# Kernel optimization log

Measured on AMD Instinct MI355X. Metric: run time of the kernel, lower is better.

The kernel has to match this reference:

```python
import jax, jax.numpy as jnp
import numpy as np

N_NODES, N_EDGES, MAX_NB = 40000, 80000, 4
INPUT_SIZE, NODE_FDIM, HIDDEN = 384, 256, 256
DEPTH = 6


def setup_inputs() -> dict:
    key = jax.random.key(0)
    ks = jax.random.split(key, 16)
    s = 0.05  # weight init scale
    return {
        "fnode": jax.random.normal(ks[0], (N_NODES, NODE_FDIM), dtype=jnp.float32),
        "fmess": jax.random.normal(ks[1], (N_EDGES, INPUT_SIZE), dtype=jnp.float32),
        "agraph": jax.random.randint(ks[2], (N_NODES, MAX_NB), 0, N_EDGES),
        "bgraph": jax.random.randint(ks[3], (N_EDGES, MAX_NB), 0, N_EDGES),
        "mask": jnp.ones((N_NODES, 1), dtype=jnp.float32),
        "Wz": jax.random.normal(ks[4], (INPUT_SIZE + HIDDEN, HIDDEN), dtype=jnp.float32) * s,
        "bz": jnp.zeros((HIDDEN,), dtype=jnp.float32),
        "Wr": jax.random.normal(ks[5], (INPUT_SIZE, HIDDEN), dtype=jnp.float32) * s,
        "Ur": jax.random.normal(ks[6], (HIDDEN, HIDDEN), dtype=jnp.float32) * s,
        "bur": jnp.zeros((HIDDEN,), dtype=jnp.float32),
        "Wh": jax.random.normal(ks[7], (INPUT_SIZE + HIDDEN, HIDDEN), dtype=jnp.float32) * s,
        "bh": jnp.zeros((HIDDEN,), dtype=jnp.float32),
        "Wo": jax.random.normal(ks[8], (NODE_FDIM + HIDDEN, HIDDEN), dtype=jnp.float32) * s,
        "bo": jnp.zeros((HIDDEN,), dtype=jnp.float32),
        "depth": DEPTH,
    }


def reference(fnode, fmess, agraph, bgraph, mask, Wz, bz, Wr, Ur, bur, Wh, bh, Wo, bo, depth):
    E, H = fmess.shape[0], Wz.shape[1]
    # message 0 is padding -> kept at zero each step (mask[0,0]=0 in torch GRU)
    msg_mask = jnp.ones((E, 1), dtype=fmess.dtype).at[0, 0].set(0.0)
    rx = fmess @ Wr  # precomputable: [E, H], reset gate input term

    def step(h, _):
        h_nei = h[bgraph]                      # [E, nb, H] gather
        sum_h = h_nei.sum(axis=1)              # [E, H]
        z = jax.nn.sigmoid(jnp.concatenate([fmess, sum_h], axis=1) @ Wz + bz)
        r = jax.nn.sigmoid(rx[:, None, :] + h_nei @ Ur + bur)  # [E, nb, H]
        sum_gh = (r * h_nei).sum(axis=1)
        pre_h = jnp.tanh(jnp.concatenate([fmess, sum_gh], axis=1) @ Wh + bh)
        h_new = ((1.0 - z) * sum_h + z * pre_h) * msg_mask
        return h_new, None

    h0 = jnp.zeros((E, H), dtype=fmess.dtype)
    h, _ = jax.lax.scan(step, h0, None, length=depth)

    nei_message = h[agraph].sum(axis=1)        # [N, H] gather-sum over incoming edges
    node_hiddens = jax.nn.relu(jnp.concatenate([fnode, nei_message], axis=1) @ Wo + bo)
    return node_hiddens * mask, h
```

## Files before the change

### kernel.cpp

```cpp
#include <hip/hip_runtime.h>
#include <stdint.h>

#define N_NODES 40000
#define N_EDGES 80000
#define HID 256
#define HC_LD 512
#define DEPTH_FIXED 6
#define NPAD 40064
#define MT 16

typedef __bf16 bf16;
typedef __bf16 bf16x4 __attribute__((ext_vector_type(4)));
typedef __bf16 bf16x8 __attribute__((ext_vector_type(8)));
typedef float f32x4 __attribute__((ext_vector_type(4)));

#define TPAD 136
#define APAD 264

__device__ __forceinline__ float sigmoidf_(float x) { return 1.f / (1.f + __expf(-x)); }
__device__ __forceinline__ float tanhf_(float x) { float e = __expf(2.f * x); return 1.f - 2.f / (e + 1.f); }

__device__ __forceinline__ void gld_lds16(const void* g, void* l) {
    __builtin_amdgcn_global_load_lds(
        (const __attribute__((address_space(1))) uint32_t*)g,
        (__attribute__((address_space(3))) uint32_t*)l, 16, 0, 0);
}

__device__ __forceinline__ void stage_tile(const bf16* __restrict__ src, int ld, int r0, int k0,
                                           bf16* lds, int tid) {
#pragma unroll
    for (int jj = 0; jj < 2; ++jj) {
        int s = jj * 256 + tid;
        int c = s ^ ((s >> 3) & 3);
        gld_lds16(src + (size_t)(r0 + (c >> 2)) * ld + k0 + (c & 3) * 8, lds + s * 8);
    }
}

__device__ __forceinline__ void mfma_tile(const bf16* lds_a, const bf16* lds_b,
                                          int wm, int wn, int lane, f32x4 (&acc)[4][4]) {
    const int li = lane & 15, quad = lane >> 4;
    const int sw = quad ^ ((li >> 1) & 3);
    bf16x8 a[4], b[4];
#pragma unroll
    for (int i = 0; i < 4; ++i)
        a[i] = *(const bf16x8*)(lds_a + ((wm * 64 + i * 16 + li) * 4 + sw) * 8);
#pragma unroll
    for (int j = 0; j < 4; ++j)
        b[j] = *(const bf16x8*)(lds_b + ((wn * 64 + j * 16 + li) * 4 + sw) * 8);
#pragma unroll
    for (int i = 0; i < 4; ++i)
#pragma unroll
        for (int j = 0; j < 4; ++j)
            acc[i][j] = __builtin_amdgcn_mfma_f32_16x16x32_bf16(a[i], b[j], acc[i][j], 0, 0, 0);
}

__global__ __launch_bounds__(256, 3) void step_fused_k(
    const int* __restrict__ bgraph, const bf16* __restrict__ HC,
    const bf16* __restrict__ P,
    const bf16* __restrict__ B1T, const bf16* __restrict__ B2T,
    bf16* __restrict__ HCn, float* __restrict__ HF) {
    __shared__ __align__(16) bf16 sA1[MT * APAD];
    __shared__ __align__(16) bf16 sA2[MT * APAD];
    __shared__ __align__(16) bf16 sBst[2 * 8192];
    const int tid = threadIdx.x, lane = tid & 63, wave = tid >> 6;
    const int m0 = blockIdx.x * MT;
    const int li = lane & 15, quad = lane >> 4;

#pragma unroll
    for (int v = 0; v < 2; ++v) {
#pragma unroll
        for (int jj = 0; jj < 4; ++jj) {
            int s = wave * 256 + jj * 64 + lane;
            int c = s ^ ((s >> 3) & 3);
            gld_lds16(B1T + (size_t)(c >> 2) * 256 + v * 32 + (c & 3) * 8,
                      sBst + v * 8192 + s * 8);
        }
    }

    {
        const int r = tid >> 4, qc = tid & 15;
        const int e = m0 + r;
        const int4 nb = *(const int4*)(bgraph + (size_t)e * 4);
        const int bi[4] = {nb.x, nb.y, nb.z, nb.w};
        const bf16* prx = P + (size_t)e * 768 + qc * 16;
        bf16x8 rx[2];
        rx[0] = *(const bf16x8*)(prx);
        rx[1] = *(const bf16x8*)(prx + 8);
        float sh[2][8] = {}, gh[2][8] = {};
#pragma unroll
        for (int p = 0; p < 2; ++p) {
            bf16x8 hv[2][2], uv[2][2];
#pragma unroll
            for (int jj = 0; jj < 2; ++jj) {
                const bf16* hp = HC + (size_t)bi[p * 2 + jj] * HC_LD + qc * 16;
                hv[jj][0] = *(const bf16x8*)(hp);
                hv[jj][1] = *(const bf16x8*)(hp + 8);
                uv[jj][0] = *(const bf16x8*)(hp + 256);
                uv[jj][1] = *(const bf16x8*)(hp + 256 + 8);
            }
#pragma unroll
            for (int jj = 0; jj < 2; ++jj)
#pragma unroll
                for (int c = 0; c < 2; ++c)
#pragma unroll
                    for (int u = 0; u < 8; ++u) {
                        float hf = (float)hv[jj][c][u];
                        float rr = sigmoidf_((float)rx[c][u] + (float)uv[jj][c][u]);
                        sh[c][u] += hf;
                        gh[c][u] += rr * hf;
                    }
        }
#pragma unroll
        for (int c = 0; c < 2; ++c) {
            bf16x8 os, og;
#pragma unroll
            for (int u = 0; u < 8; ++u) { os[u] = (bf16)sh[c][u]; og[u] = (bf16)gh[c][u]; }
            *(bf16x8*)(sA1 + r * APAD + qc * 16 + c * 8) = os;
            *(bf16x8*)(sA2 + r * APAD + qc * 16 + c * 8) = og;
        }
    }
    __syncthreads();

    const int sw = quad ^ ((li >> 1) & 3);
    f32x4 accZ[4] = {}, accH[4] = {};
#pragma unroll
    for (int u = 0; u < 16; ++u) {
        if (u < 15) { asm volatile("s_waitcnt vmcnt(4)" ::: "memory"); }
        else        { asm volatile("s_waitcnt vmcnt(0)" ::: "memory"); }
        __builtin_amdgcn_sched_barrier(0);
        const bf16* sA = (u < 8) ? sA1 : sA2;
        const int t = u & 7;
        bf16x8 a = *(const bf16x8*)(sA + li * APAD + t * 32 + quad * 8);
        bf16x8 b[4];
#pragma unroll
        for (int j = 0; j < 4; ++j)
            b[j] = *(const bf16x8*)(sBst + (u & 1) * 8192 + ((wave * 64 + j * 16 + li) * 4 + sw) * 8);
        asm volatile("s_waitcnt lgkmcnt(0)" ::: "memory");
        __builtin_amdgcn_sched_barrier(0);
        const int v = u + 2;
        if (v < 16) {
            const bf16* BTn = (v < 8) ? B1T : B2T;
            const int tn = v & 7;
#pragma unroll
            for (int jj = 0; jj < 4; ++jj) {
                int s = wave * 256 + jj * 64 + lane;
                int c = s ^ ((s >> 3) & 3);
                gld_lds16(BTn + (size_t)(c >> 2) * 256 + tn * 32 + (c & 3) * 8,
                          sBst + (u & 1) * 8192 + s * 8);
            }
        }
#pragma unroll
        for (int j = 0; j < 4; ++j) {
            if (u < 8) accZ[j] = __builtin_amdgcn_mfma_f32_16x16x32_bf16(a, b[j], accZ[j], 0, 0, 0);
            else       accH[j] = __builtin_amdgcn_mfma_f32_16x16x32_bf16(a, b[j], accH[j], 0, 0, 0);
        }
    }

    __syncthreads();

    bf16* tZ = sA2;
    bf16* tH = sBst;
#pragma unroll
    for (int j = 0; j < 4; ++j) {
        const int col = wave * 64 + j * 16 + li;
#pragma unroll
        for (int r = 0; r < 4; ++r) {
            const int row = quad * 4 + r;
            tZ[row * APAD + col] = (bf16)accZ[j][r];
            tH[row * 256 + col] = (bf16)accH[j][r];
        }
    }
    __syncthreads();
#pragma unroll
    for (int s = 0; s < 2; ++s) {
        int v = s * 256 + tid;
        int lr = v >> 5, c8 = (v & 31) * 8;
        int e = m0 + lr;
        bf16x8 zl = *(const bf16x8*)(tZ + lr * APAD + c8);
        bf16x8 hl = *(const bf16x8*)(tH + lr * 256 + c8);
        bf16x8 shv = *(const bf16x8*)(sA1 + lr * APAD + c8);
        bf16x8 zx = *(const bf16x8*)(P + (size_t)e * 768 + 256 + c8);
        bf16x8 hx = *(const bf16x8*)(P + (size_t)e * 768 + 512 + c8);
        bf16x8 o;
        float of[8];
#pragma unroll
        for (int u = 0; u < 8; ++u) {
            float z = sigmoidf_((float)zl[u] + (float)zx[u]);
            float p = tanhf_((float)hl[u] + (float)hx[u]);
            float hn = (1.f - z) * (float)shv[u] + z * p;
            if (e == 0) hn = 0.f;
            o[u] = (bf16)hn;
            of[u] = hn;
        }
        *(bf16x8*)(HCn + (size_t)e * HC_LD + c8) = o;
        if (HF) {
            *(float4*)(HF + (size_t)e * HID + c8) = make_float4(of[0], of[1], of[2], of[3]);
            *(float4*)(HF + (size_t)e * HID + c8 + 4) = make_float4(of[4], of[5], of[6], of[7]);
        }
    }
}

__global__ __launch_bounds__(256) void gemm_single_k(
    const bf16* __restrict__ A, int lda, const bf16* __restrict__ BT,
    const float* __restrict__ bias, bf16* __restrict__ C, int K, int ldc) {
    __shared__ __align__(16) char smem[34816];
    bf16* sA = (bf16*)smem;
    bf16* sB = sA + 4096;
    const int tid = threadIdx.x, lane = tid & 63, wave = tid >> 6;
    const int wm = wave >> 1, wn = wave & 1;
    const int m0 = blockIdx.x * 128, n0 = blockIdx.y * 128;
    f32x4 acc[4][4] = {};
    for (int k0 = 0; k0 < K; k0 += 32) {
        stage_tile(A, lda, m0, k0, sA, tid);
        stage_tile(BT, K, n0, k0, sB, tid);
        __syncthreads();
        mfma_tile(sA, sB, wm, wn, lane, acc);
        __syncthreads();
    }
    bf16* tC = (bf16*)smem;
#pragma unroll
    for (int i = 0; i < 4; ++i)
#pragma unroll
        for (int j = 0; j < 4; ++j) {
            const int col = wn * 64 + j * 16 + (lane & 15);
#pragma unroll
            for (int r = 0; r < 4; ++r) {
                const int lr = wm * 64 + i * 16 + (lane >> 4) * 4 + r;
                tC[lr * TPAD + col] = (bf16)acc[i][j][r];
            }
        }
    __syncthreads();
#pragma unroll
    for (int s = 0; s < 8; ++s) {
        int v = s * 256 + tid;
        int lr = v >> 4, c8 = (v & 15) * 8;
        bf16x8 cv = *(const bf16x8*)(tC + lr * TPAD + c8);
        bf16x8 o;
        if (bias) {
            float4 b0 = *(const float4*)(bias + n0 + c8);
            float4 b1 = *(const float4*)(bias + n0 + c8 + 4);
            o[0] = (bf16)((float)cv[0] + b0.x); o[1] = (bf16)((float)cv[1] + b0.y);
            o[2] = (bf16)((float)cv[2] + b0.z); o[3] = (bf16)((float)cv[3] + b0.w);
            o[4] = (bf16)((float)cv[4] + b1.x); o[5] = (bf16)((float)cv[5] + b1.y);
            o[6] = (bf16)((float)cv[6] + b1.z); o[7] = (bf16)((float)cv[7] + b1.w);
        } else {
            o = cv;
        }
        *(bf16x8*)(C + (size_t)(m0 + lr) * ldc + n0 + c8) = o;
    }
}

__global__ __launch_bounds__(256) void gemm_out_k(
    const bf16* __restrict__ A1, const bf16* __restrict__ A2,
    const bf16* __restrict__ B1T, const bf16* __restrict__ B2T,
    const float* __restrict__ bo, const float* __restrict__ mask, float* __restrict__ out) {
    __shared__ __align__(16) char smem[34816];
    bf16* s0 = (bf16*)smem;
    bf16* s1 = s0 + 4096;
    bf16* s2 = s1 + 4096;
    bf16* s3 = s2 + 4096;
    const int tid = threadIdx.x, lane = tid & 63, wave = tid >> 6;
    const int wm = wave >> 1, wn = wave & 1;
    const int m0 = blockIdx.x * 128, n0 = blockIdx.y * 128;
    f32x4 acc1[4][4] = {}, acc2[4][4] = {};
    for (int k0 = 0; k0 < 256; k0 += 32) {
        stage_tile(A1, 256, m0, k0, s0, tid);
        stage_tile(B1T, 256, n0, k0, s1, tid);
        stage_tile(A2, 256, m0, k0, s2, tid);
        stage_tile(B2T, 256, n0, k0, s3, tid);
        __syncthreads();
        mfma_tile(s0, s1, wm, wn, lane, acc1);
        mfma_tile(s2, s3, wm, wn, lane, acc2);
        __syncthreads();
    }
    bf16* tC = (bf16*)smem;
#pragma unroll
    for (int i = 0; i < 4; ++i)
#pragma unroll
        for (int j = 0; j < 4; ++j) {
            const int col = wn * 64 + j * 16 + (lane & 15);
#pragma unroll
            for (int r = 0; r < 4; ++r) {
                const int lr = wm * 64 + i * 16 + (lane >> 4) * 4 + r;
                tC[lr * TPAD + col] = (bf16)(acc1[i][j][r] + acc2[i][j][r]);
            }
        }
    __syncthreads();
#pragma unroll
    for (int s = 0; s < 8; ++s) {
        int v = s * 256 + tid;
        int lr = v >> 4, c8 = (v & 15) * 8;
        int grow = m0 + lr;
        if (grow >= N_NODES) continue;
        int gcol = n0 + c8;
        bf16x8 cv = *(const bf16x8*)(tC + lr * TPAD + c8);
        float4 b0 = *(const float4*)(bo + gcol);
        float4 b1 = *(const float4*)(bo + gcol + 4);
        float mk = mask[grow];
        float4 o0, o1;
        o0.x = fmaxf((float)cv[0] + b0.x, 0.f) * mk;
        o0.y = fmaxf((float)cv[1] + b0.y, 0.f) * mk;
        o0.z = fmaxf((float)cv[2] + b0.z, 0.f) * mk;
        o0.w = fmaxf((float)cv[3] + b0.w, 0.f) * mk;
        o1.x = fmaxf((float)cv[4] + b1.x, 0.f) * mk;
        o1.y = fmaxf((float)cv[5] + b1.y, 0.f) * mk;
        o1.z = fmaxf((float)cv[6] + b1.z, 0.f) * mk;
        o1.w = fmaxf((float)cv[7] + b1.w, 0.f) * mk;
        *(float4*)(out + (size_t)grow * 256 + gcol) = o0;
        *(float4*)(out + (size_t)grow * 256 + gcol + 4) = o1;
    }
}

__global__ __launch_bounds__(256) void gather_nei_k(
    const int* __restrict__ agraph, const bf16* __restrict__ H, bf16* __restrict__ nei) {
    int i = blockIdx.x * 256 + threadIdx.x;
    int v = i >> 5, c8 = (i & 31) * 8;
    bf16x8 o;
    if (v < N_NODES) {
        int4 nb = *(const int4*)(agraph + (size_t)v * 4);
        int bi[4] = {nb.x, nb.y, nb.z, nb.w};
        float s[8] = {};
#pragma unroll
        for (int j = 0; j < 4; ++j) {
            bf16x8 hv = *(const bf16x8*)(H + (size_t)bi[j] * HC_LD + c8);
#pragma unroll
            for (int r = 0; r < 8; ++r) s[r] += (float)hv[r];
        }
#pragma unroll
        for (int r = 0; r < 8; ++r) o[r] = (bf16)s[r];
    } else {
#pragma unroll
        for (int r = 0; r < 8; ++r) o[r] = (bf16)0.f;
    }
    *(bf16x8*)(nei + (size_t)v * HID + c8) = o;
}

__global__ __launch_bounds__(256) void step1_k(const bf16* __restrict__ P, bf16* __restrict__ HC) {
    int i = blockIdx.x * 256 + threadIdx.x;
    int e = i >> 5, c8 = (i & 31) * 8;
    bf16x8 zx = *(const bf16x8*)(P + (size_t)e * 768 + 256 + c8);
    bf16x8 hx = *(const bf16x8*)(P + (size_t)e * 768 + 512 + c8);
    bf16x8 o;
#pragma unroll
    for (int r = 0; r < 8; ++r) {
        float h = sigmoidf_((float)zx[r]) * tanhf_((float)hx[r]);
        if (e == 0) h = 0.f;
        o[r] = (bf16)h;
    }
    *(bf16x8*)(HC + (size_t)e * HC_LD + c8) = o;
}

__global__ void cvt_bf16_k(const float* __restrict__ src, bf16* __restrict__ dst, int n4) {
    int i = blockIdx.x * 256 + threadIdx.x;
    if (i >= n4) return;
    float4 v = ((const float4*)src)[i];
    bf16x4 o = {(bf16)v.x, (bf16)v.y, (bf16)v.z, (bf16)v.w};
    *((bf16x4*)dst + i) = o;
}

__global__ void cvt_fnode_k(const float* __restrict__ src, bf16* __restrict__ dst) {
    int i = blockIdx.x * 256 + threadIdx.x;
    int row = i >> 6;
    bf16x4 o = {(bf16)0.f, (bf16)0.f, (bf16)0.f, (bf16)0.f};
    if (row < N_NODES) {
        float4 v = ((const float4*)src)[i];
        o[0] = (bf16)v.x; o[1] = (bf16)v.y; o[2] = (bf16)v.z; o[3] = (bf16)v.w;
    }
    *((bf16x4*)dst + i) = o;
}

__global__ void prep_wpre_k(const float* __restrict__ Wr, const float* __restrict__ Wz,
                            const float* __restrict__ Wh, bf16* __restrict__ WT) {
    int idx = blockIdx.x * 256 + threadIdx.x;
    if (idx >= 768 * 384) return;
    int n = idx / 384, k = idx % 384;
    float v;
    if (n < 256) v = Wr[(size_t)k * 256 + n];
    else if (n < 512) v = Wz[(size_t)k * 256 + (n - 256)];
    else v = Wh[(size_t)k * 256 + (n - 512)];
    WT[idx] = (bf16)v;
}

__global__ void prep_bias_k(const float* __restrict__ bur, const float* __restrict__ bz,
                            const float* __restrict__ bh, float* __restrict__ bp) {
    int n = blockIdx.x * 256 + threadIdx.x;
    if (n >= 768) return;
    bp[n] = n < 256 ? bur[n] : (n < 512 ? bz[n - 256] : bh[n - 512]);
}

__global__ void prep_t256_k(const float* __restrict__ W, bf16* __restrict__ T, int roff) {
    int idx = blockIdx.x * 256 + threadIdx.x;
    int n = idx >> 8, k = idx & 255;
    T[idx] = (bf16)W[(size_t)(roff + k) * 256 + n];
}

extern "C" void kernel_launch(void* const* d_in, const int* in_sizes, int n_in,
                              void* d_out, int out_size, void* d_ws, size_t ws_size,
                              hipStream_t stream) {
    (void)in_sizes; (void)n_in; (void)out_size; (void)ws_size;
    const float* fnode = (const float*)d_in[0];
    const float* fmess = (const float*)d_in[1];
    const int* agraph = (const int*)d_in[2];
    const int* bgraph = (const int*)d_in[3];
    const float* mask = (const float*)d_in[4];
    const float* Wz = (const float*)d_in[5];
    const float* bz = (const float*)d_in[6];
    const float* Wr = (const float*)d_in[7];
    const float* Ur = (const float*)d_in[8];
    const float* bur = (const float*)d_in[9];
    const float* Wh = (const float*)d_in[10];
    const float* bh = (const float*)d_in[11];
    const float* Wo = (const float*)d_in[12];
    const float* bo = (const float*)d_in[13];
    float* out_node = (float*)d_out;
    float* out_h = out_node + (size_t)N_NODES * HID;

    char* ws = (char*)d_ws;
    size_t off = 0;
    auto alloc = [&](size_t b) -> char* { char* p = ws + off; off += (b + 255) & ~(size_t)255; return p; };
    bf16* P     = (bf16*)alloc((size_t)N_EDGES * 768 * 2);
    bf16* HC0   = (bf16*)alloc((size_t)N_EDGES * HC_LD * 2);
    bf16* HC1   = (bf16*)alloc((size_t)N_EDGES * HC_LD * 2);
    bf16* fnodeB= (bf16*)alloc((size_t)NPAD * HID * 2);
    bf16* nei   = (bf16*)alloc((size_t)NPAD * HID * 2);
    bf16* WTpre = (bf16*)alloc((size_t)768 * 384 * 2);
    bf16* UrT   = (bf16*)alloc(65536 * 2);
    bf16* WzBT  = (bf16*)alloc(65536 * 2);
    bf16* WhBT  = (bf16*)alloc(65536 * 2);
    bf16* WoTT  = (bf16*)alloc(65536 * 2);
    bf16* WoBT  = (bf16*)alloc(65536 * 2);
    float* biasP= (float*)alloc(768 * 4);
    bf16* fmessB = HC1;

    cvt_bf16_k<<<30000, 256, 0, stream>>>(fmess, fmessB, N_EDGES * 384 / 4);
    cvt_fnode_k<<<NPAD * 64 / 256, 256, 0, stream>>>(fnode, fnodeB);
    prep_wpre_k<<<(768 * 384 + 255) / 256, 256, 0, stream>>>(Wr, Wz, Wh, WTpre);
    prep_bias_k<<<3, 256, 0, stream>>>(bur, bz, bh, biasP);
    prep_t256_k<<<256, 256, 0, stream>>>(Ur, UrT, 0);
    prep_t256_k<<<256, 256, 0, stream>>>(Wz, WzBT, 384);
    prep_t256_k<<<256, 256, 0, stream>>>(Wh, WhBT, 384);
    prep_t256_k<<<256, 256, 0, stream>>>(Wo, WoTT, 0);
    prep_t256_k<<<256, 256, 0, stream>>>(Wo, WoBT, 256);

    gemm_single_k<<<dim3(625, 6), 256, 0, stream>>>(fmessB, 384, WTpre, biasP, P, 384, 768);

    step1_k<<<N_EDGES * 32 / 256, 256, 0, stream>>>(P, HC0);

    bf16* cur = HC0;
    bf16* nxt = HC1;
    for (int d = 2; d <= DEPTH_FIXED; ++d) {
        gemm_single_k<<<dim3(625, 2), 256, 0, stream>>>(cur, HC_LD, UrT, nullptr, cur + 256, 256, HC_LD);
        step_fused_k<<<N_EDGES / MT, 256, 0, stream>>>(bgraph, cur, P, WzBT, WhBT, nxt,
                                                       d == DEPTH_FIXED ? out_h : nullptr);
        bf16* t = cur; cur = nxt; nxt = t;
    }

    gather_nei_k<<<NPAD * 32 / 256, 256, 0, stream>>>(agraph, cur, nei);
    gemm_out_k<<<dim3(313, 2), 256, 0, stream>>>(fnodeB, nei, WoTT, WoBT, bo, mask, out_node);
}
```

Before: 1.232 ms.

## Double step kernel edge tile to 32 rows with 8 waves per block

The fused GRU step kernel now processes 32 edges per block with 512 threads. Each of the 8 waves owns a 32-column slice and computes a 2x2 grid of MFMA tiles, so every weight tile streamed into shared memory is reused across twice as many edges. The neighbour gather now issues all four neighbour row loads before any arithmetic, which raises memory-level parallelism. In exchange it uses more registers, and the larger blocks may lower occupancy and leave fewer blocks to spread across the GPU.

```diff
diff --git a/kernel.cpp b/kernel.cpp
--- a/kernel.cpp
+++ b/kernel.cpp
@@ -7,7 +7,7 @@
 #define HC_LD 512
 #define DEPTH_FIXED 6
 #define NPAD 40064
-#define MT 16
+#define MT 32
 
 typedef __bf16 bf16;
 typedef __bf16 bf16x4 __attribute__((ext_vector_type(4)));
@@ -54,7 +54,7 @@
             acc[i][j] = __builtin_amdgcn_mfma_f32_16x16x32_bf16(a[i], b[j], acc[i][j], 0, 0, 0);
 }
 
-__global__ __launch_bounds__(256, 3) void step_fused_k(
+__global__ __launch_bounds__(512, 2) void step_fused_k(
     const int* __restrict__ bgraph, const bf16* __restrict__ HC,
     const bf16* __restrict__ P,
     const bf16* __restrict__ B1T, const bf16* __restrict__ B2T,
@@ -69,11 +69,11 @@
 #pragma unroll
     for (int v = 0; v < 2; ++v) {
 #pragma unroll
-        for (int jj = 0; jj < 4; ++jj) {
-            int s = wave * 256 + jj * 64 + lane;
+        for (int jj = 0; jj < 2; ++jj) {
+            int s = jj * 64 + lane;
             int c = s ^ ((s >> 3) & 3);
-            gld_lds16(B1T + (size_t)(c >> 2) * 256 + v * 32 + (c & 3) * 8,
-                      sBst + v * 8192 + s * 8);
+            gld_lds16(B1T + (size_t)(wave * 32 + (c >> 2)) * 256 + v * 32 + (c & 3) * 8,
+                      sBst + v * 8192 + wave * 1024 + s * 8);
         }
     }
 
@@ -86,30 +86,27 @@
         bf16x8 rx[2];
         rx[0] = *(const bf16x8*)(prx);
         rx[1] = *(const bf16x8*)(prx + 8);
+        bf16x8 hv[4][2], uv[4][2];
+#pragma unroll
+        for (int j = 0; j < 4; ++j) {
+            const bf16* hp = HC + (size_t)bi[j] * HC_LD + qc * 16;
+            hv[j][0] = *(const bf16x8*)(hp);
+            hv[j][1] = *(const bf16x8*)(hp + 8);
+            uv[j][0] = *(const bf16x8*)(hp + 256);
+            uv[j][1] = *(const bf16x8*)(hp + 256 + 8);
+        }
         float sh[2][8] = {}, gh[2][8] = {};
 #pragma unroll
-        for (int p = 0; p < 2; ++p) {
-            bf16x8 hv[2][2], uv[2][2];
-#pragma unroll
-            for (int jj = 0; jj < 2; ++jj) {
-                const bf16* hp = HC + (size_t)bi[p * 2 + jj] * HC_LD + qc * 16;
-                hv[jj][0] = *(const bf16x8*)(hp);
-                hv[jj][1] = *(const bf16x8*)(hp + 8);
-                uv[jj][0] = *(const bf16x8*)(hp + 256);
-                uv[jj][1] = *(const bf16x8*)(hp + 256 + 8);
-            }
-#pragma unroll
-            for (int jj = 0; jj < 2; ++jj)
-#pragma unroll
-                for (int c = 0; c < 2; ++c)
-#pragma unroll
-                    for (int u = 0; u < 8; ++u) {
-                        float hf = (float)hv[jj][c][u];
-                        float rr = sigmoidf_((float)rx[c][u] + (float)uv[jj][c][u]);
-                        sh[c][u] += hf;
-                        gh[c][u] += rr * hf;
-                    }
-        }
+        for (int j = 0; j < 4; ++j)
+#pragma unroll
+            for (int c = 0; c < 2; ++c)
+#pragma unroll
+                for (int u = 0; u < 8; ++u) {
+                    float hf = (float)hv[j][c][u];
+                    float rr = sigmoidf_((float)rx[c][u] + (float)uv[j][c][u]);
+                    sh[c][u] += hf;
+                    gh[c][u] += rr * hf;
+                }
 #pragma unroll
         for (int c = 0; c < 2; ++c) {
             bf16x8 os, og;
@@ -122,19 +119,21 @@
     __syncthreads();
 
     const int sw = quad ^ ((li >> 1) & 3);
-    f32x4 accZ[4] = {}, accH[4] = {};
+    f32x4 accZ[2][2] = {}, accH[2][2] = {};
 #pragma unroll
     for (int u = 0; u < 16; ++u) {
-        if (u < 15) { asm volatile("s_waitcnt vmcnt(4)" ::: "memory"); }
+        if (u < 15) { asm volatile("s_waitcnt vmcnt(2)" ::: "memory"); }
         else        { asm volatile("s_waitcnt vmcnt(0)" ::: "memory"); }
         __builtin_amdgcn_sched_barrier(0);
         const bf16* sA = (u < 8) ? sA1 : sA2;
         const int t = u & 7;
-        bf16x8 a = *(const bf16x8*)(sA + li * APAD + t * 32 + quad * 8);
-        bf16x8 b[4];
-#pragma unroll
-        for (int j = 0; j < 4; ++j)
-            b[j] = *(const bf16x8*)(sBst + (u & 1) * 8192 + ((wave * 64 + j * 16 + li) * 4 + sw) * 8);
+        bf16x8 a[2], b[2];
+#pragma unroll
+        for (int i = 0; i < 2; ++i)
+            a[i] = *(const bf16x8*)(sA + (i * 16 + li) * APAD + t * 32 + quad * 8);
+#pragma unroll
+        for (int j = 0; j < 2; ++j)
+            b[j] = *(const bf16x8*)(sBst + (u & 1) * 8192 + wave * 1024 + ((j * 16 + li) * 4 + sw) * 8);
         asm volatile("s_waitcnt lgkmcnt(0)" ::: "memory");
         __builtin_amdgcn_sched_barrier(0);
         const int v = u + 2;
@@ -142,18 +141,20 @@
             const bf16* BTn = (v < 8) ? B1T : B2T;
             const int tn = v & 7;
 #pragma unroll
-            for (int jj = 0; jj < 4; ++jj) {
-                int s = wave * 256 + jj * 64 + lane;
+            for (int jj = 0; jj < 2; ++jj) {
+                int s = jj * 64 + lane;
                 int c = s ^ ((s >> 3) & 3);
-                gld_lds16(BTn + (size_t)(c >> 2) * 256 + tn * 32 + (c & 3) * 8,
-                          sBst + (u & 1) * 8192 + s * 8);
+                gld_lds16(BTn + (size_t)(wave * 32 + (c >> 2)) * 256 + tn * 32 + (c & 3) * 8,
+                          sBst + (u & 1) * 8192 + wave * 1024 + s * 8);
             }
         }
 #pragma unroll
-        for (int j = 0; j < 4; ++j) {
-            if (u < 8) accZ[j] = __builtin_amdgcn_mfma_f32_16x16x32_bf16(a, b[j], accZ[j], 0, 0, 0);
-            else       accH[j] = __builtin_amdgcn_mfma_f32_16x16x32_bf16(a, b[j], accH[j], 0, 0, 0);
-        }
+        for (int i = 0; i < 2; ++i)
+#pragma unroll
+            for (int j = 0; j < 2; ++j) {
+                if (u < 8) accZ[i][j] = __builtin_amdgcn_mfma_f32_16x16x32_bf16(a[i], b[j], accZ[i][j], 0, 0, 0);
+                else       accH[i][j] = __builtin_amdgcn_mfma_f32_16x16x32_bf16(a[i], b[j], accH[i][j], 0, 0, 0);
+            }
     }
 
     __syncthreads();
@@ -161,19 +162,21 @@
     bf16* tZ = sA2;
     bf16* tH = sBst;
 #pragma unroll
-    for (int j = 0; j < 4; ++j) {
-        const int col = wave * 64 + j * 16 + li;
-#pragma unroll
-        for (int r = 0; r < 4; ++r) {
-            const int row = quad * 4 + r;
-            tZ[row * APAD + col] = (bf16)accZ[j][r];
-            tH[row * 256 + col] = (bf16)accH[j][r];
-        }
-    }
+    for (int i = 0; i < 2; ++i)
+#pragma unroll
+        for (int j = 0; j < 2; ++j) {
+            const int col = wave * 32 + j * 16 + li;
+#pragma unroll
+            for (int r = 0; r < 4; ++r) {
+                const int row = i * 16 + quad * 4 + r;
+                tZ[row * APAD + col] = (bf16)accZ[i][j][r];
+                tH[row * 256 + col] = (bf16)accH[i][j][r];
+            }
+        }
     __syncthreads();
 #pragma unroll
     for (int s = 0; s < 2; ++s) {
-        int v = s * 256 + tid;
+        int v = s * 512 + tid;
         int lr = v >> 5, c8 = (v & 31) * 8;
         int e = m0 + lr;
         bf16x8 zl = *(const bf16x8*)(tZ + lr * APAD + c8);
@@ -450,7 +453,7 @@
     bf16* nxt = HC1;
     for (int d = 2; d <= DEPTH_FIXED; ++d) {
         gemm_single_k<<<dim3(625, 2), 256, 0, stream>>>(cur, HC_LD, UrT, nullptr, cur + 256, 256, HC_LD);
-        step_fused_k<<<N_EDGES / MT, 256, 0, stream>>>(bgraph, cur, P, WzBT, WhBT, nxt,
+        step_fused_k<<<N_EDGES / MT, 512, 0, stream>>>(bgraph, cur, P, WzBT, WhBT, nxt,
                                                        d == DEPTH_FIXED ? out_h : nullptr);
         bf16* t = cur; cur = nxt; nxt = t;
     }
```

Measured after the change: 1.292 ms. +4.9%, slower.
